# Optimization experiments

Measured on AMD Instinct MI355X. Metric: run time of the kernel, lower is better.

## Reference

```python
import jax, jax.numpy as jnp
import numpy as np

N = 648      # code length (input_size = output_size)
DV = 3       # variable degree
DC = 6       # check degree
M_PER = N // DC            # checks per layer = 108
E = N * DV                 # edges = hidden_size = 1944
BATCH = 2048
CLAMP = 0.999999


def _build_graph():
    rng = np.random.default_rng(0)
    # regular (3,6) Tanner graph via 3 permutation layers
    var_of = np.concatenate([rng.permutation(N) for _ in range(DV)])          # [E]
    chk_of = np.repeat(np.arange(DV * M_PER), DC)                              # [E]
    eye = np.eye(E, dtype=bool)
    same_chk = (chk_of[:, None] == chk_of[None, :]) & ~eye                     # extrinsic same-check
    same_var = (var_of[:, None] == var_of[None, :]) & ~eye                     # extrinsic same-var
    M_ev = np.zeros((E, N), dtype=np.float32)
    M_ev[np.arange(E), var_of] = 1.0                                           # edge -> its variable
    M_first = (same_chk.astype(np.float32) @ M_ev)                             # [E,N] CN extrinsic over vars
    M_cn = same_chk.astype(np.float32)                                         # [E,E] VN2CN_mask_CNUpdate
    M_vn = same_var.astype(np.float32)                                         # [E,E] CN2VN_mask_VNUpdate
    M_out = M_ev.T.copy()                                                      # [N,E] CN2VN_mask_output
    bias_matrix = M_ev.T.copy()                                                # [N,E] dot_bias_matrix
    return M_first, M_cn, M_vn, M_out, bias_matrix


def _xavier(key, out_f, in_f, mask):
    bound = np.sqrt(6.0 / (in_f + out_f)).astype(np.float32)
    w = jax.random.uniform(key, (out_f, in_f), jnp.float32, -bound, bound)
    return w * mask


def setup_inputs() -> dict:
    key = jax.random.key(0)
    M_first, M_cn, M_vn, M_out, bias_matrix = _build_graph()
    M_first = jnp.asarray(M_first); M_cn = jnp.asarray(M_cn)
    M_vn = jnp.asarray(M_vn); M_out = jnp.asarray(M_out)
    bias_matrix = jnp.asarray(bias_matrix)
    ks = jax.random.split(key, 6)
    x = jax.random.normal(ks[0], (BATCH, N), jnp.float32) * 2.0  # channel LLRs
    W1 = _xavier(ks[1], E, E, M_vn)
    W3 = _xavier(ks[2], E, E, M_vn)
    W5 = _xavier(ks[3], E, E, M_vn)
    W7 = _xavier(ks[4], E, E, M_vn)
    W9 = _xavier(ks[5], N, E, M_out)
    B0 = jnp.eye(N, dtype=jnp.float32); B1 = jnp.eye(N, dtype=jnp.float32)
    B2 = jnp.eye(N, dtype=jnp.float32); B3 = jnp.eye(N, dtype=jnp.float32)
    B4 = jnp.eye(N, dtype=jnp.float32)
    return {"x": x, "M_first": M_first, "M_cn": M_cn, "M_out": M_out,
            "bias_matrix": bias_matrix, "W1": W1, "W3": W3, "W5": W5,
            "W7": W7, "W9": W9, "B0": B0, "B1": B1, "B2": B2, "B3": B3, "B4": B4}


def cn_update(x, mask):
    """out[b,i] = prod over j with mask[i,j]!=0 and x[b,j]!=0 of x[b,j]; 0 if none.
    Computed in sign/log domain so it is three dense [B,in]@[in,out] matmuls
    instead of a Python loop over rows."""
    nz = x != 0.0
    logmag = jnp.log(jnp.where(nz, jnp.abs(x), 1.0))          # 0 contribution where x==0
    neg = (x < 0.0).astype(x.dtype)
    log_prod = logmag @ mask.T                                 # [B,out]
    neg_cnt = neg @ mask.T
    sign = 1.0 - 2.0 * jnp.mod(neg_cnt, 2.0)
    any_nz = (nz.astype(x.dtype) @ mask.T) > 0.0
    return jnp.where(any_nz, sign * jnp.exp(log_prod), 0.0)


def reference(x, M_first, M_cn, M_out, bias_matrix, W1, W3, W5, W7, W9,
              B0, B1, B2, B3, B4):
    llr = x                                                    # Channel_LLR [B,N]
    t = jnp.tanh(0.5 * x)
    t = jnp.clip(cn_update(t, M_first), -CLAMP, CLAMP)
    t = 2.0 * jnp.arctanh(t)
    out1 = jax.nn.sigmoid(t @ M_out.T + llr)                   # count_loss_fc: ones*mask weight, zero bias

    t = jnp.tanh(0.5 * (t @ W1.T + (llr @ B0) @ bias_matrix))
    t = jnp.clip(cn_update(t, M_cn), -CLAMP, CLAMP)
    t = 2.0 * jnp.arctanh(t)
    out2 = jax.nn.sigmoid(t @ M_out.T + llr)

    t = jnp.tanh(0.5 * (t @ W3.T + (llr @ B1) @ bias_matrix))
    t = jnp.clip(cn_update(t, M_cn), -CLAMP, CLAMP)
    t = 2.0 * jnp.arctanh(t)
    out3 = jax.nn.sigmoid(t @ M_out.T + llr)

    t = jnp.tanh(0.5 * (t @ W5.T + (llr @ B2) @ bias_matrix))
    t = jnp.clip(cn_update(t, M_cn), -CLAMP, CLAMP)
    t = 2.0 * jnp.arctanh(t)
    out4 = jax.nn.sigmoid(t @ M_out.T + llr)

    t = jnp.tanh(0.5 * (t @ W7.T + (llr @ B3) @ bias_matrix))
    t = jnp.clip(cn_update(t, M_cn), -CLAMP, CLAMP)
    t = 2.0 * jnp.arctanh(t)
    t = t @ W9.T + llr @ B4
    out5 = jax.nn.sigmoid(t)
    return (out5, out4, out3, out2, out1)
```

## Files before the change

### kernel.cpp

```cpp
#include <hip/hip_runtime.h>
#include <math.h>

#define NN 648
#define EE 1944
#define NP 972
#define BATCH 2048
#define BS 256
#define NP_IT 4
#define TL_CLAMP 14.508648f

__device__ __forceinline__ float rcp_fast(float x) { return __builtin_amdgcn_rcpf(x); }

__device__ __forceinline__ float tanh_half(float x) {
    float E = __expf(x);
    float big = 1.0f - 2.0f * rcp_fast(E + 1.0f);
    float u = 0.5f * x;
    float small = u * (1.0f - 0.33333334f * u * u);
    return (fabsf(x) < 0.03125f) ? small : big;
}

__device__ __forceinline__ float sigm(float s) {
    return rcp_fast(1.0f + __expf(-s));
}

__device__ __noinline__ float cn_fallback(float a, const float2 v01,
                                          const float2 v23, const float2 v45) {
    float vv[6] = {v01.x, v01.y, v23.x, v23.y, v45.x, v45.y};
    float P = 1.0f; int cz = 0;
    #pragma unroll
    for (int k = 0; k < 6; k++) {
        if (vv[k] == 0.0f) cz++; else P *= vv[k];
    }
    float ext;
    if (a != 0.0f) ext = (cz >= 5) ? 0.0f : P * rcp_fast(a);
    else           ext = (cz >= 6) ? 0.0f : P;
    ext = fminf(fmaxf(ext, -0.999999f), 0.999999f);
    return 0.6931472f * __log2f((1.0f + ext) * rcp_fast(1.0f - ext));
}

__device__ __forceinline__ float cn_edge(float a, float Q) {
    float t = 0.6931472f * (__log2f(fabsf(a + Q)) - __log2f(fabsf(a - Q)));
    return fminf(fmaxf(t, -TL_CLAMP), TL_CLAMP);
}

__global__ __launch_bounds__(BS) void extract_struct(
    const float4* __restrict__ M_out4,
    int* __restrict__ var_of, int* __restrict__ varEdge) {
    int t = blockIdx.x * BS + threadIdx.x;
    if (t >= NN * EE / 4) return;
    float4 v = M_out4[t];
    int flat = t * 4;
    int n = flat / EE;
    int e = flat - n * EE;
    if (v.x != 0.0f) { var_of[e]     = n; varEdge[n * 3 + (e)     / NN] = e;     }
    if (v.y != 0.0f) { var_of[e + 1] = n; varEdge[n * 3 + (e + 1) / NN] = e + 1; }
    if (v.z != 0.0f) { var_of[e + 2] = n; varEdge[n * 3 + (e + 2) / NN] = e + 2; }
    if (v.w != 0.0f) { var_of[e + 3] = n; varEdge[n * 3 + (e + 3) / NN] = e + 3; }
}

__global__ __launch_bounds__(BS) void extract_weights(
    const float* __restrict__ W1, const float* __restrict__ W3,
    const float* __restrict__ W5, const float* __restrict__ W7,
    const float* __restrict__ W9,
    const int* __restrict__ var_of, const int* __restrict__ varEdge,
    int4* __restrict__ nbq,
    float4* __restrict__ w1q, float4* __restrict__ w3q,
    float4* __restrict__ w5q, float4* __restrict__ w7q,
    float* __restrict__ w9v) {
    int t = blockIdx.x * BS + threadIdx.x;
    if (t < 4 * EE) {
        int m = t / EE;
        int e = t - m * EE;
        int n = var_of[e];
        int e0 = varEdge[3 * n], e1 = varEdge[3 * n + 1], e2 = varEdge[3 * n + 2];
        int ea, eb;
        if (e == e0)      { ea = e1; eb = e2; }
        else if (e == e1) { ea = e0; eb = e2; }
        else              { ea = e0; eb = e1; }
        const float* W = (m == 0) ? W1 : (m == 1) ? W3 : (m == 2) ? W5 : W7;
        size_t row = (size_t)e * EE;
        float2 w = make_float2(W[row + ea], W[row + eb]);
        float4* dq = (m == 0) ? w1q : (m == 1) ? w3q : (m == 2) ? w5q : w7q;
        ((float2*)dq)[e] = w;
        if (m == 0) ((int2*)nbq)[e] = make_int2(ea, eb);
    } else if (t < 4 * EE + NN) {
        int n = t - 4 * EE;
        #pragma unroll
        for (int k = 0; k < 3; k++) {
            int e = varEdge[3 * n + k];
            w9v[3 * n + k] = W9[(size_t)n * EE + e];
        }
    }
}

__global__ __launch_bounds__(BS, 8) void bp_main(
    const float* __restrict__ x,
    const int2* __restrict__ var2,
    const int* __restrict__ varEdge,
    const int4* __restrict__ nbq,
    const float4* __restrict__ w1q, const float4* __restrict__ w3q,
    const float4* __restrict__ w5q, const float4* __restrict__ w7q,
    const float* __restrict__ w9v,
    float* __restrict__ out) {
    __shared__ __align__(16) float llr_s[NN];
    __shared__ __align__(16) float te[EE];
    __shared__ __align__(16) float tl[EE];
    const int b = blockIdx.x;
    const int tid = threadIdx.x;

    const float* xr = x + (size_t)b * NN;
    for (int n = tid; n < NN; n += BS) llr_s[n] = xr[n];
    __syncthreads();

    float2 lb[NP_IT];
    int oA[NP_IT], oB[NP_IT], oC[NP_IT], oD[NP_IT];
    int cOff[NP_IT];
    #pragma unroll
    for (int i = 0; i < NP_IT; i++) {
        int p = tid + i * BS;
        if (p < NP) {
            int2 v = var2[p];
            lb[i] = make_float2(llr_s[v.x], llr_s[v.y]);
            int4 nn = nbq[p];
            oA[i] = nn.x; oB[i] = nn.y; oC[i] = nn.z; oD[i] = nn.w;
            cOff[i] = ((unsigned)p / 3u) * 6;
            *(float2*)(te + 2 * p) = make_float2(tanh_half(lb[i].x),
                                                 tanh_half(lb[i].y));
        } else {
            lb[i] = make_float2(0.f, 0.f);
            oA[i] = oB[i] = oC[i] = oD[i] = 0; cOff[i] = 0;
        }
    }
    int m0[3], m1[3], m2[3];
    #pragma unroll
    for (int j = 0; j < 3; j++) {
        int n = tid + j * BS;
        if (n < NN) {
            m0[j] = varEdge[3 * n]; m1[j] = varEdge[3 * n + 1];
            m2[j] = varEdge[3 * n + 2];
        } else { m0[j] = m1[j] = m2[j] = 0; }
    }
    __syncthreads();

    auto cn_pass = [&]() {
        #pragma unroll
        for (int i = 0; i < NP_IT; i++) {
            int p = tid + i * BS;
            if (p >= NP) break;
            const float2* ck = (const float2*)(te + cOff[i]);
            float2 v01 = ck[0], v23 = ck[1], v45 = ck[2];
            float2 a = *(const float2*)(te + 2 * p);
            float Q = ((v01.x * v01.y) * (v23.x * v23.y)) * (v45.x * v45.y);
            float t0, t1;
            if (__builtin_expect(Q != 0.0f, 1)) {
                t0 = cn_edge(a.x, Q);
                t1 = cn_edge(a.y, Q);
            } else {
                t0 = cn_fallback(a.x, v01, v23, v45);
                t1 = cn_fallback(a.y, v01, v23, v45);
            }
            *(float2*)(tl + 2 * p) = make_float2(t0, t1);
        }
    };
    auto marg_out = [&](float* dst) {
        #pragma unroll
        for (int j = 0; j < 3; j++) {
            int n = tid + j * BS;
            if (n < NN)
                dst[n] = sigm(llr_s[n] + tl[m0[j]] + tl[m1[j]] + tl[m2[j]]);
        }
    };

    cn_pass();
    __syncthreads();
    marg_out(out + ((size_t)(4 * BATCH) + b) * NN);

    const float4* wqs[4] = {w1q, w3q, w5q, w7q};
    for (int L = 0; L < 4; L++) {
        const float4* __restrict__ wq = wqs[L];
        #pragma unroll
        for (int i = 0; i < NP_IT; i++) {
            int p = tid + i * BS;
            if (p < NP) {
                float4 w = wq[p];
                float preX = fmaf(w.x, tl[oA[i]], fmaf(w.y, tl[oB[i]], lb[i].x));
                float preY = fmaf(w.z, tl[oC[i]], fmaf(w.w, tl[oD[i]], lb[i].y));
                *(float2*)(te + 2 * p) = make_float2(tanh_half(preX),
                                                     tanh_half(preY));
            }
        }
        __syncthreads();
        cn_pass();
        __syncthreads();
        if (L < 3) {
            marg_out(out + ((size_t)((3 - L) * BATCH) + b) * NN);
        } else {
            #pragma unroll
            for (int j = 0; j < 3; j++) {
                int n = tid + j * BS;
                if (n < NN) {
                    float s = llr_s[n]
                            + w9v[3 * n]     * tl[m0[j]]
                            + w9v[3 * n + 1] * tl[m1[j]]
                            + w9v[3 * n + 2] * tl[m2[j]];
                    out[(size_t)b * NN + n] = sigm(s);
                }
            }
        }
    }
}

extern "C" void kernel_launch(void* const* d_in, const int* in_sizes, int n_in,
                              void* d_out, int out_size, void* d_ws, size_t ws_size,
                              hipStream_t stream) {
    const float* x     = (const float*)d_in[0];
    const float* M_out = (const float*)d_in[3];
    const float* W1    = (const float*)d_in[5];
    const float* W3    = (const float*)d_in[6];
    const float* W5    = (const float*)d_in[7];
    const float* W7    = (const float*)d_in[8];
    const float* W9    = (const float*)d_in[9];
    float* out = (float*)d_out;

    char* ws = (char*)d_ws;
    int4*   nbq     = (int4*)ws;   ws += NP * 16;
    float4* w1q     = (float4*)ws; ws += NP * 16;
    float4* w3q     = (float4*)ws; ws += NP * 16;
    float4* w5q     = (float4*)ws; ws += NP * 16;
    float4* w7q     = (float4*)ws; ws += NP * 16;
    int*    var_of  = (int*)ws;    ws += EE * 4;
    int*    varEdge = (int*)ws;    ws += NN * 3 * 4;
    float*  w9v     = (float*)ws;  ws += NN * 3 * 4;

    const int tot4 = NN * EE / 4;
    extract_struct<<<(tot4 + BS - 1) / BS, BS, 0, stream>>>(
        (const float4*)M_out, var_of, varEdge);
    const int totW = 4 * EE + NN;
    extract_weights<<<(totW + BS - 1) / BS, BS, 0, stream>>>(
        W1, W3, W5, W7, W9, var_of, varEdge, nbq, w1q, w3q, w5q, w7q, w9v);
    bp_main<<<BATCH, BS, 0, stream>>>(
        x, (const int2*)var_of, varEdge, nbq, w1q, w3q, w5q, w7q, w9v, out);
}
```

Before: 175.7 us.

## Assign one thread per check node, keep check messages in registers

The main kernel now maps each of the 324 check nodes to one thread, with blocks of 384 threads. Each thread holds its six edge tanh values, neighbor indices and channel LLRs in registers. This drops the shared-memory te array and one __syncthreads per layer, and ping-pongs between two shared tl buffers so the update reads the old layer while writing the new one. Indices are packed into 16-bit halves to cut index loads. In exchange, per-thread register use rises and 60 of the 384 threads sit idle during the check phase.

```diff
diff --git a/kernel.cpp b/kernel.cpp
--- a/kernel.cpp
+++ b/kernel.cpp
@@ -3,10 +3,10 @@
 
 #define NN 648
 #define EE 1944
-#define NP 972
+#define NCHK 324
 #define BATCH 2048
 #define BS 256
-#define NP_IT 4
+#define BSM 384
 #define TL_CLAMP 14.508648f
 
 __device__ __forceinline__ float rcp_fast(float x) { return __builtin_amdgcn_rcpf(x); }
@@ -23,9 +23,14 @@
     return rcp_fast(1.0f + __expf(-s));
 }
 
-__device__ __noinline__ float cn_fallback(float a, const float2 v01,
-                                          const float2 v23, const float2 v45) {
-    float vv[6] = {v01.x, v01.y, v23.x, v23.y, v45.x, v45.y};
+__device__ __forceinline__ float cn_edge(float a, float Q) {
+    float t = 0.6931472f * (__log2f(fabsf(a + Q)) - __log2f(fabsf(a - Q)));
+    return fminf(fmaxf(t, -TL_CLAMP), TL_CLAMP);
+}
+
+__device__ __noinline__ float cn_fallback(float a, float t0, float t1, float t2,
+                                          float t3, float t4, float t5) {
+    float vv[6] = {t0, t1, t2, t3, t4, t5};
     float P = 1.0f; int cz = 0;
     #pragma unroll
     for (int k = 0; k < 6; k++) {
@@ -38,24 +43,20 @@
     return 0.6931472f * __log2f((1.0f + ext) * rcp_fast(1.0f - ext));
 }
 
-__device__ __forceinline__ float cn_edge(float a, float Q) {
-    float t = 0.6931472f * (__log2f(fabsf(a + Q)) - __log2f(fabsf(a - Q)));
-    return fminf(fmaxf(t, -TL_CLAMP), TL_CLAMP);
-}
-
 __global__ __launch_bounds__(BS) void extract_struct(
     const float4* __restrict__ M_out4,
-    int* __restrict__ var_of, int* __restrict__ varEdge) {
+    int* __restrict__ var_of, int* __restrict__ varEdge,
+    unsigned short* __restrict__ varc16) {
     int t = blockIdx.x * BS + threadIdx.x;
     if (t >= NN * EE / 4) return;
     float4 v = M_out4[t];
     int flat = t * 4;
     int n = flat / EE;
     int e = flat - n * EE;
-    if (v.x != 0.0f) { var_of[e]     = n; varEdge[n * 3 + (e)     / NN] = e;     }
-    if (v.y != 0.0f) { var_of[e + 1] = n; varEdge[n * 3 + (e + 1) / NN] = e + 1; }
-    if (v.z != 0.0f) { var_of[e + 2] = n; varEdge[n * 3 + (e + 2) / NN] = e + 2; }
-    if (v.w != 0.0f) { var_of[e + 3] = n; varEdge[n * 3 + (e + 3) / NN] = e + 3; }
+    if (v.x != 0.0f) { var_of[e]     = n; varEdge[n*3 + (e)    /NN] = e;     varc16[e]     = (unsigned short)n; }
+    if (v.y != 0.0f) { var_of[e + 1] = n; varEdge[n*3 + (e + 1)/NN] = e + 1; varc16[e + 1] = (unsigned short)n; }
+    if (v.z != 0.0f) { var_of[e + 2] = n; varEdge[n*3 + (e + 2)/NN] = e + 2; varc16[e + 2] = (unsigned short)n; }
+    if (v.w != 0.0f) { var_of[e + 3] = n; varEdge[n*3 + (e + 3)/NN] = e + 3; varc16[e + 3] = (unsigned short)n; }
 }
 
 __global__ __launch_bounds__(BS) void extract_weights(
@@ -63,7 +64,7 @@
     const float* __restrict__ W5, const float* __restrict__ W7,
     const float* __restrict__ W9,
     const int* __restrict__ var_of, const int* __restrict__ varEdge,
-    int4* __restrict__ nbq,
+    unsigned* __restrict__ nb6,
     float4* __restrict__ w1q, float4* __restrict__ w3q,
     float4* __restrict__ w5q, float4* __restrict__ w7q,
     float* __restrict__ w9v) {
@@ -82,7 +83,7 @@
         float2 w = make_float2(W[row + ea], W[row + eb]);
         float4* dq = (m == 0) ? w1q : (m == 1) ? w3q : (m == 2) ? w5q : w7q;
         ((float2*)dq)[e] = w;
-        if (m == 0) ((int2*)nbq)[e] = make_int2(ea, eb);
+        if (m == 0) nb6[e] = (unsigned)ea | ((unsigned)eb << 16);
     } else if (t < 4 * EE + NN) {
         int n = t - 4 * EE;
         #pragma unroll
@@ -93,116 +94,111 @@
     }
 }
 
-__global__ __launch_bounds__(BS, 8) void bp_main(
+__global__ __launch_bounds__(BSM, 8) void bp_main(
     const float* __restrict__ x,
-    const int2* __restrict__ var2,
+    const unsigned* __restrict__ varc,
+    const unsigned* __restrict__ nb6,
     const int* __restrict__ varEdge,
-    const int4* __restrict__ nbq,
     const float4* __restrict__ w1q, const float4* __restrict__ w3q,
     const float4* __restrict__ w5q, const float4* __restrict__ w7q,
     const float* __restrict__ w9v,
     float* __restrict__ out) {
     __shared__ __align__(16) float llr_s[NN];
-    __shared__ __align__(16) float te[EE];
-    __shared__ __align__(16) float tl[EE];
+    __shared__ __align__(16) float tlA[EE];
+    __shared__ __align__(16) float tlB[EE];
     const int b = blockIdx.x;
     const int tid = threadIdx.x;
 
-    const float* xr = x + (size_t)b * NN;
-    for (int n = tid; n < NN; n += BS) llr_s[n] = xr[n];
+    {
+        const float2* xr2 = (const float2*)(x + (size_t)b * NN);
+        if (tid < NN / 2) ((float2*)llr_s)[tid] = xr2[tid];
+    }
     __syncthreads();
 
-    float2 lb[NP_IT];
-    int oA[NP_IT], oB[NP_IT], oC[NP_IT], oD[NP_IT];
-    int cOff[NP_IT];
+    const bool ck = tid < NCHK;
+    const int c = tid;
+    float lb[6];
+    unsigned nbp[6];
+    float te[6];
+
+    if (ck) {
+        #pragma unroll
+        for (int j = 0; j < 3; j++) {
+            unsigned vv = varc[3 * c + j];
+            lb[2 * j]     = llr_s[vv & 0xffffu];
+            lb[2 * j + 1] = llr_s[vv >> 16];
+        }
+        #pragma unroll
+        for (int j = 0; j < 6; j++) {
+            nbp[j] = nb6[6 * c + j];
+            te[j] = tanh_half(lb[j]);
+        }
+    }
+    int m0[2], m1[2], m2[2];
     #pragma unroll
-    for (int i = 0; i < NP_IT; i++) {
-        int p = tid + i * BS;
-        if (p < NP) {
-            int2 v = var2[p];
-            lb[i] = make_float2(llr_s[v.x], llr_s[v.y]);
-            int4 nn = nbq[p];
-            oA[i] = nn.x; oB[i] = nn.y; oC[i] = nn.z; oD[i] = nn.w;
-            cOff[i] = ((unsigned)p / 3u) * 6;
-            *(float2*)(te + 2 * p) = make_float2(tanh_half(lb[i].x),
-                                                 tanh_half(lb[i].y));
-        } else {
-            lb[i] = make_float2(0.f, 0.f);
-            oA[i] = oB[i] = oC[i] = oD[i] = 0; cOff[i] = 0;
-        }
-    }
-    int m0[3], m1[3], m2[3];
-    #pragma unroll
-    for (int j = 0; j < 3; j++) {
-        int n = tid + j * BS;
+    for (int j = 0; j < 2; j++) {
+        int n = tid + j * BSM;
         if (n < NN) {
             m0[j] = varEdge[3 * n]; m1[j] = varEdge[3 * n + 1];
             m2[j] = varEdge[3 * n + 2];
         } else { m0[j] = m1[j] = m2[j] = 0; }
     }
-    __syncthreads();
-
-    auto cn_pass = [&]() {
-        #pragma unroll
-        for (int i = 0; i < NP_IT; i++) {
-            int p = tid + i * BS;
-            if (p >= NP) break;
-            const float2* ck = (const float2*)(te + cOff[i]);
-            float2 v01 = ck[0], v23 = ck[1], v45 = ck[2];
-            float2 a = *(const float2*)(te + 2 * p);
-            float Q = ((v01.x * v01.y) * (v23.x * v23.y)) * (v45.x * v45.y);
-            float t0, t1;
-            if (__builtin_expect(Q != 0.0f, 1)) {
-                t0 = cn_edge(a.x, Q);
-                t1 = cn_edge(a.y, Q);
-            } else {
-                t0 = cn_fallback(a.x, v01, v23, v45);
-                t1 = cn_fallback(a.y, v01, v23, v45);
-            }
-            *(float2*)(tl + 2 * p) = make_float2(t0, t1);
+
+    auto cn_store = [&](float* dst) {
+        float Q = ((te[0] * te[1]) * (te[2] * te[3])) * (te[4] * te[5]);
+        float* d = dst + 6 * c;
+        if (__builtin_expect(Q != 0.0f, 1)) {
+            #pragma unroll
+            for (int j = 0; j < 6; j++) d[j] = cn_edge(te[j], Q);
+        } else {
+            #pragma unroll
+            for (int j = 0; j < 6; j++)
+                d[j] = cn_fallback(te[j], te[0], te[1], te[2], te[3], te[4], te[5]);
         }
     };
-    auto marg_out = [&](float* dst) {
-        #pragma unroll
-        for (int j = 0; j < 3; j++) {
-            int n = tid + j * BS;
+    auto marg = [&](const float* tl, float* dst) {
+        #pragma unroll
+        for (int j = 0; j < 2; j++) {
+            int n = tid + j * BSM;
             if (n < NN)
                 dst[n] = sigm(llr_s[n] + tl[m0[j]] + tl[m1[j]] + tl[m2[j]]);
         }
     };
 
-    cn_pass();
+    if (ck) cn_store(tlA);
     __syncthreads();
-    marg_out(out + ((size_t)(4 * BATCH) + b) * NN);
+    marg(tlA, out + ((size_t)(4 * BATCH) + b) * NN);
 
     const float4* wqs[4] = {w1q, w3q, w5q, w7q};
+    #pragma unroll
     for (int L = 0; L < 4; L++) {
         const float4* __restrict__ wq = wqs[L];
-        #pragma unroll
-        for (int i = 0; i < NP_IT; i++) {
-            int p = tid + i * BS;
-            if (p < NP) {
-                float4 w = wq[p];
-                float preX = fmaf(w.x, tl[oA[i]], fmaf(w.y, tl[oB[i]], lb[i].x));
-                float preY = fmaf(w.z, tl[oC[i]], fmaf(w.w, tl[oD[i]], lb[i].y));
-                *(float2*)(te + 2 * p) = make_float2(tanh_half(preX),
-                                                     tanh_half(preY));
+        const float* tlc = (L & 1) ? tlB : tlA;
+        float* tln = (L & 1) ? tlA : tlB;
+        if (ck) {
+            float4 wa = wq[3 * c], wb = wq[3 * c + 1], wc = wq[3 * c + 2];
+            float w[12] = {wa.x, wa.y, wa.z, wa.w, wb.x, wb.y, wb.z, wb.w,
+                           wc.x, wc.y, wc.z, wc.w};
+            #pragma unroll
+            for (int j = 0; j < 6; j++) {
+                float pre = fmaf(w[2 * j], tlc[nbp[j] & 0xffffu],
+                            fmaf(w[2 * j + 1], tlc[nbp[j] >> 16], lb[j]));
+                te[j] = tanh_half(pre);
             }
-        }
-        __syncthreads();
-        cn_pass();
+            cn_store(tln);
+        }
         __syncthreads();
         if (L < 3) {
-            marg_out(out + ((size_t)((3 - L) * BATCH) + b) * NN);
+            marg(tln, out + ((size_t)((3 - L) * BATCH) + b) * NN);
         } else {
             #pragma unroll
-            for (int j = 0; j < 3; j++) {
-                int n = tid + j * BS;
+            for (int j = 0; j < 2; j++) {
+                int n = tid + j * BSM;
                 if (n < NN) {
                     float s = llr_s[n]
-                            + w9v[3 * n]     * tl[m0[j]]
-                            + w9v[3 * n + 1] * tl[m1[j]]
-                            + w9v[3 * n + 2] * tl[m2[j]];
+                            + w9v[3 * n]     * tln[m0[j]]
+                            + w9v[3 * n + 1] * tln[m1[j]]
+                            + w9v[3 * n + 2] * tln[m2[j]];
                     out[(size_t)b * NN + n] = sigm(s);
                 }
             }
@@ -223,21 +219,22 @@
     float* out = (float*)d_out;
 
     char* ws = (char*)d_ws;
-    int4*   nbq     = (int4*)ws;   ws += NP * 16;
-    float4* w1q     = (float4*)ws; ws += NP * 16;
-    float4* w3q     = (float4*)ws; ws += NP * 16;
-    float4* w5q     = (float4*)ws; ws += NP * 16;
-    float4* w7q     = (float4*)ws; ws += NP * 16;
-    int*    var_of  = (int*)ws;    ws += EE * 4;
-    int*    varEdge = (int*)ws;    ws += NN * 3 * 4;
-    float*  w9v     = (float*)ws;  ws += NN * 3 * 4;
+    float4* w1q     = (float4*)ws;         ws += (EE / 2) * 16;
+    float4* w3q     = (float4*)ws;         ws += (EE / 2) * 16;
+    float4* w5q     = (float4*)ws;         ws += (EE / 2) * 16;
+    float4* w7q     = (float4*)ws;         ws += (EE / 2) * 16;
+    int*    var_of  = (int*)ws;            ws += EE * 4;
+    int*    varEdge = (int*)ws;            ws += NN * 3 * 4;
+    float*  w9v     = (float*)ws;          ws += NN * 3 * 4;
+    unsigned* nb6   = (unsigned*)ws;       ws += EE * 4;
+    unsigned short* varc16 = (unsigned short*)ws; ws += EE * 2;
 
     const int tot4 = NN * EE / 4;
     extract_struct<<<(tot4 + BS - 1) / BS, BS, 0, stream>>>(
-        (const float4*)M_out, var_of, varEdge);
+        (const float4*)M_out, var_of, varEdge, varc16);
     const int totW = 4 * EE + NN;
     extract_weights<<<(totW + BS - 1) / BS, BS, 0, stream>>>(
-        W1, W3, W5, W7, W9, var_of, varEdge, nbq, w1q, w3q, w5q, w7q, w9v);
-    bp_main<<<BATCH, BS, 0, stream>>>(
-        x, (const int2*)var_of, varEdge, nbq, w1q, w3q, w5q, w7q, w9v, out);
-}
+        W1, W3, W5, W7, W9, var_of, varEdge, nb6, w1q, w3q, w5q, w7q, w9v);
+    bp_main<<<BATCH, BSM, 0, stream>>>(
+        x, (const unsigned*)varc16, nb6, varEdge, w1q, w3q, w5q, w7q, w9v, out);
+}
```

Measured after the change: 166.3 us. 1.06x faster.
